# Optimization experiments

Hardware: AMD Instinct MI355X
Metric: run time of the kernel (lower is better)

## Reference

```python
import jax, jax.numpy as jnp
import numpy as np

B, NCH, T = 16, 64, 15000
WS, ST = 500, 250
SR = 250.0
EPS = 1e-06
DM = 512
LN_EPS = 1e-05


def _spectral_constants():
    freqs = np.fft.rfftfreq(WS, d=1.0 / SR).astype(np.float32)  # [F]
    bands = [(1.0, 4.0), (4.0, 8.0), (8.0, 13.0), (13.0, 30.0)]
    bm = np.stack([(freqs >= lo) & (freqs < hi) for lo, hi in bands]).astype(np.float32)  # [4, F]
    bm_norm = bm / bm.sum(axis=1, keepdims=True)  # mean over band bins == matmul with normalized mask
    alpha = ((freqs >= 7.0) & (freqs <= 13.5)).astype(np.float32)  # [F]
    return jnp.asarray(freqs), jnp.asarray(bm_norm), jnp.asarray(alpha)

FREQS, BAND_MASK_NORM, ALPHA_MASK = _spectral_constants()
NUM_FRAMES = (T - WS) // ST + 1
FRAME_IDX = np.arange(NUM_FRAMES)[:, None] * ST + np.arange(WS)[None, :]  # [W, WS]


def _linear_params(k, fin, fout):
    kw, kb = jax.random.split(k)
    W = jax.random.normal(kw, (fin, fout), jnp.float32) * 0.02
    b = jax.random.normal(kb, (fout,), jnp.float32) * 0.01
    return W, b


def setup_inputs() -> dict:
    key = jax.random.key(0)
    ks = jax.random.split(key, 8)
    x = jax.random.normal(ks[0], (B, NCH, T), jnp.float32)
    sensor_pos = jax.random.normal(ks[1], (B, NCH, 2), jnp.float32) * 0.1
    sensor_mask = jax.random.bernoulli(ks[2], 0.9, (B, NCH))
    IN_F = 4 * 3 + 3   # 15
    IN_D = 4 * 2 + 3   # 11
    Wf1, bf1 = _linear_params(ks[3], IN_F, DM)
    Wf2, bf2 = _linear_params(ks[4], DM, DM)
    Wd1, bd1 = _linear_params(ks[5], IN_D, DM)
    Wd2, bd2 = _linear_params(ks[6], DM, DM)
    ln_g = jnp.ones((DM,), jnp.float32)
    ln_b = jnp.zeros((DM,), jnp.float32)
    return {"x": x, "sensor_pos": sensor_pos, "sensor_mask": sensor_mask,
            "Wf1": Wf1, "bf1": bf1, "Wf2": Wf2, "bf2": bf2,
            "ln_g": ln_g, "ln_b": ln_b,
            "Wd1": Wd1, "bd1": bd1, "Wd2": Wd2, "bd2": bd2}


def _mlp(z, W1, b1, W2, b2):
    h = jax.nn.gelu(z @ W1 + b1, approximate=False)
    return h @ W2 + b2


def _layernorm(z, g, b):
    mu = z.mean(-1, keepdims=True)
    var = jnp.var(z, axis=-1, keepdims=True)
    return (z - mu) * jax.lax.rsqrt(var + LN_EPS) * g + b


def _safe_mask(v, fallback):
    return jnp.where(v.any(), v, jnp.full_like(v, fallback))


def _forward(x, sensor_pos, sensor_mask, Wf1, bf1, Wf2, bf2, ln_g, ln_b, Wd1, bd1, Wd2, bd2):
    # frames: [B, W, C, WS]
    frames = x[:, :, FRAME_IDX].transpose(0, 2, 1, 3)
    frames = frames - frames.mean(-1, keepdims=True)
    valid = sensor_mask.astype(frames.dtype)[:, None, :, None]  # [B,1,C,1]
    frames = frames * valid
    spec = jnp.fft.rfft(frames.astype(jnp.float32), axis=-1)
    power = jnp.abs(spec) ** 2 + EPS  # [B,W,C,F]

    # masked band-power means via normalized mask matmul -> [B,W,C,4]
    band_power_t = jnp.einsum('bwcf,kf->bwck', power, BAND_MASK_NORM)
    total_power = jnp.maximum(band_power_t.sum(-1, keepdims=True), EPS)
    rel_power = band_power_t / total_power

    valid_ch = valid  # [B,1,C,1]
    ch_cnt = jnp.maximum(valid_ch.sum(2, keepdims=True), 1.0)
    chan_mean = (band_power_t * valid_ch).sum(2, keepdims=True) / ch_cnt
    topo_dev = jnp.log(jnp.maximum(band_power_t, EPS)) - jnp.log(jnp.maximum(chan_mean, EPS))

    pos_x = sensor_pos[..., 0]
    pos_y = sensor_pos[..., 1]
    left = _safe_mask((pos_x < -0.02) & sensor_mask, False)
    right = _safe_mask((pos_x > 0.02) & sensor_mask, False)
    posterior = _safe_mask((pos_y < -0.02) & sensor_mask, True)
    anterior = _safe_mask((pos_y > 0.02) & sensor_mask, False)

    alpha_power = band_power_t[..., 2]  # [B,W,C]

    def region_mean(m):  # m: [B,C] bool -> [B,W]
        cnt = jnp.maximum(m.sum(-1).astype(alpha_power.dtype), 1.0)[:, None]
        return (alpha_power * m.astype(alpha_power.dtype)[:, None, :]).sum(-1) / cnt

    left_a, right_a = region_mean(left), region_mean(right)
    post_a, ant_a = region_mean(posterior), region_mean(anterior)
    alpha_asym = (left_a - right_a) / jnp.maximum(left_a + right_a + EPS, EPS)
    alpha_ap = (post_a - ant_a) / jnp.maximum(post_a + ant_a + EPS, EPS)
    support = (anterior.sum(-1) > 0) & (posterior.sum(-1) > 0)  # [B]
    alpha_ap = jnp.where(support[:, None], alpha_ap, jnp.zeros_like(alpha_ap))

    alpha_spec = power * ALPHA_MASK  # [B,W,C,F]
    alpha_sum = jnp.maximum(alpha_spec.sum(-1), EPS)
    alpha_peak_freq = (alpha_spec * FREQS).sum(-1) / alpha_sum  # [B,W,C]
    alpha_peak_score = alpha_spec.max(-1) / jnp.maximum(power.mean(-1), EPS)

    log_power = jnp.log(jnp.maximum(band_power_t, EPS))
    channel_ap = jnp.broadcast_to(sensor_pos[:, None, :, 1], alpha_peak_freq.shape)

    features = jnp.concatenate([
        log_power, rel_power, topo_dev,
        alpha_peak_freq[..., None], alpha_peak_score[..., None], channel_ap[..., None],
    ], axis=-1)  # [B,W,C,15]

    ch_cnt2 = jnp.maximum(valid_ch.sum(2), 1.0)  # [B,1,1]
    band_mean = (band_power_t * valid_ch).sum(2) / ch_cnt2       # [B,W,4]
    band_rel_mean = (rel_power * valid_ch).sum(2) / ch_cnt2      # [B,W,4]
    band_log_mean = jnp.log(jnp.maximum(band_mean, EPS))
    delta_theta = band_rel_mean[..., 0] + band_rel_mean[..., 1]
    desc = jnp.concatenate([
        band_log_mean, band_rel_mean,
        jnp.stack([alpha_asym, alpha_ap, delta_theta], axis=-1),
    ], axis=-1)  # [B,W,11]

    tokens = _layernorm(_mlp(features.astype(x.dtype), Wf1, bf1, Wf2, bf2), ln_g, ln_b)
    desc_out = _mlp(desc.astype(x.dtype), Wd1, bd1, Wd2, bd2)
    return tokens, desc_out


def reference(x, sensor_pos, sensor_mask, Wf1, bf1, Wf2, bf2, ln_g, ln_b, Wd1, bd1, Wd2, bd2):
    return _forward(x, sensor_pos, sensor_mask, Wf1, bf1, Wf2, bf2, ln_g, ln_b, Wd1, bd1, Wd2, bd2)
```

## Files before the change

### kernel.cpp

```cpp
#include <hip/hip_runtime.h>
#include <math.h>

#define EPS 1e-6f
#define LN_EPS 1e-5f

typedef __attribute__((ext_vector_type(8))) short bf16x8;
typedef __attribute__((ext_vector_type(4))) float f32x4;

#define SD_OFF    0ULL
#define SD_SZ     (1024ULL*60*128*4)
#define BP_OFF    SD_OFF
#define BTH_OFF   (SD_OFF + 4ULL*1024*1024)
#define BTL_OFF   (BTH_OFF + 65536ULL)
#define FEAT_OFF  (SD_OFF + SD_SZ)
#define FEAT_SZ   (60416ULL*16*4)
#define H_OFF     (FEAT_OFF + FEAT_SZ)
#define H_SZ      (60416ULL*512*2)
#define WT_OFF    (H_OFF + H_SZ)
#define WT_SZ     (512ULL*512*2)
#define DSC_OFF   (WT_OFF + WT_SZ)
#define DSC_SZ    (944ULL*16*4)
#define MSK_OFF   (DSC_OFF + DSC_SZ)
#define MSK_SZ    (1024ULL*4)
#define REG_OFF   (MSK_OFF + MSK_SZ)
#define REG_SZ    (4096ULL*4)
#define CNT_OFF   (REG_OFF + REG_SZ)
#define CNT_SZ    (64ULL*4)
#define SUP_OFF   (CNT_OFF + CNT_SZ)

#define TOKENS_N  30932992ULL

__device__ inline unsigned short f2bf(float f) {
  union { float f; unsigned u; } v; v.f = f;
  unsigned u = v.u;
  return (unsigned short)((u + 0x7fffu + ((u >> 16) & 1u)) >> 16);
}

__device__ inline void gload16(const void* g, void* l) {
  __builtin_amdgcn_global_load_lds((const __attribute__((address_space(1))) unsigned int*)g,
                                   (__attribute__((address_space(3))) unsigned int*)l, 16, 0, 0);
}

__global__ __launch_bounds__(1024) void k_setup(const void* mraw, const float* spos,
    float* maskf, float* regm, float* cnts, float* sup) {
  __shared__ int okint, okflt;
  __shared__ int anyr[4];
  __shared__ float cbuf[4][16];
  int t = threadIdx.x;
  if (t == 0) { okint = 1; okflt = 1; }
  if (t < 4) anyr[t] = 0;
  if (t < 64) cbuf[t>>4][t&15] = 0.f;
  __syncthreads();
  if (t < 256) {
    unsigned v = ((const unsigned*)mraw)[t];
    if (v > 1u) okint = 0;
    if (v != 0u && v != 0x3f800000u) okflt = 0;
  }
  __syncthreads();
  float mv;
  if (okint)      mv = (float)((const int*)mraw)[t];
  else if (okflt) mv = ((const float*)mraw)[t];
  else            mv = (float)((const unsigned char*)mraw)[t];
  maskf[t] = mv;
  bool mk = mv > 0.5f;
  float px = spos[2*t], py = spos[2*t+1];
  int lm = ((px < -0.02f) && mk) ? 1 : 0;
  int rm = ((px >  0.02f) && mk) ? 1 : 0;
  int pm = ((py < -0.02f) && mk) ? 1 : 0;
  int am = ((py >  0.02f) && mk) ? 1 : 0;
  if (lm) anyr[0] = 1;
  if (rm) anyr[1] = 1;
  if (pm) anyr[2] = 1;
  if (am) anyr[3] = 1;
  __syncthreads();
  float lv = anyr[0] ? (float)lm : 0.f;
  float rv = anyr[1] ? (float)rm : 0.f;
  float pv = anyr[2] ? (float)pm : 1.f;
  float av = anyr[3] ? (float)am : 0.f;
  regm[t] = lv; regm[1024+t] = rv; regm[2048+t] = pv; regm[3072+t] = av;
  int b = t >> 6;
  atomicAdd(&cbuf[0][b], lv);
  atomicAdd(&cbuf[1][b], rv);
  atomicAdd(&cbuf[2][b], pv);
  atomicAdd(&cbuf[3][b], av);
  __syncthreads();
  if (t < 64) cnts[t] = cbuf[t>>4][t&15];
  if (t < 16) sup[t] = (cbuf[3][t] > 0.f && cbuf[2][t] > 0.f) ? 1.f : 0.f;
}

__global__ __launch_bounds__(256) void k_wt(const float* Wf2, unsigned short* Wt) {
  __shared__ float tile[64][65];
  int tx = threadIdx.x & 63, ty = threadIdx.x >> 6;
  int k0 = blockIdx.x * 64, n0 = blockIdx.y * 64;
  for (int r = ty; r < 64; r += 4)
    tile[r][tx] = Wf2[(size_t)(k0 + r)*512 + n0 + tx];
  __syncthreads();
  for (int r = ty; r < 64; r += 4)
    Wt[(size_t)(n0 + r)*512 + k0 + tx] = f2bf(tile[tx][r]);
}

__global__ __launch_bounds__(256) void k_twid(unsigned short* FBh, unsigned short* FBl) {
  int col = blockIdx.x, k = threadIdx.x;
  float w = 0.f;
  if (k < 250) {
    if (col < 116) {
      int kk = (col >> 1) + 2;
      int km = (kk * k) % 500;
      float ang = (float)km * 0.012566370614359172f;
      w = (col & 1) ? sinf(ang) : cosf(ang);
    } else if (col == 116) w = (k & 1) ? -1.f : 1.f;
    else if (col == 117) w = 1.f;
  }
  unsigned u = __float_as_uint(w);
  float hf = __uint_as_float(u & 0xffff0000u);
  float r = w - hf;
  int ni2 = col >> 6, nf = (col >> 4) & 3, r15 = col & 15;
  int kt = k >> 5, lg4 = (k >> 3) & 3, e = k & 7;
  int idx = ((((kt*2 + ni2)*4 + nf)*64) + (lg4*16 + r15))*8 + e;
  FBh[idx] = (unsigned short)(u >> 16);
  FBl[idx] = (unsigned short)(__float_as_uint(r) >> 16);
}

__global__ __launch_bounds__(256) void k_dft(const float* __restrict__ x, const float* maskf,
    const unsigned short* __restrict__ FBh, const unsigned short* __restrict__ FBl,
    float* __restrict__ bpg) {
  int c = blockIdx.x, b = blockIdx.y;
  int bc = b*64 + c;
  __shared__ __align__(16) float xs[15360];
  __shared__ float Ep[64][4];
  int t = threadIdx.x;
  float mvv = maskf[bc];
  const float4* xp4 = (const float4*)(x + (size_t)bc*15000);
  float4* xs4 = (float4*)xs;
  for (int i = t; i < 3750; i += 256) {
    float4 v = xp4[i];
    v.x *= mvv; v.y *= mvv; v.z *= mvv; v.w *= mvv;
    xs4[i] = v;
  }
  if (t < 90) xs4[3750 + t] = make_float4(0.f, 0.f, 0.f, 0.f);
  __syncthreads();
  if (t < 240) {
    int j = t >> 2, q = t & 3;
    int len = (q < 3) ? 31 : 32;
    const float2* p = (const float2*)(xs + j*250 + q*62);
    float e = 0.f;
    for (int i = 0; i < len; ++i) { float2 v = p[i]; e = fmaf(v.x, v.x, fmaf(v.y, v.y, e)); }
    Ep[j][q] = e;
  }
  int L = t & 63, wv = t >> 6;
  int mi2 = wv >> 1, ni2 = wv & 1;
  int r15 = L & 15, lg4 = L >> 4;
  f32x4 acc[2][4];
#pragma unroll
  for (int mf = 0; mf < 2; ++mf)
#pragma unroll
    for (int nf = 0; nf < 4; ++nf) acc[mf][nf] = (f32x4){0.f,0.f,0.f,0.f};
  int rowA = mi2*32 + r15;
  const unsigned short* fbh0 = FBh + (size_t)(ni2*4*64 + L)*8;
  const unsigned short* fbl0 = FBl + (size_t)(ni2*4*64 + L)*8;
  for (int kt = 0; kt < 8; ++kt) {
    int k0 = kt*32 + lg4*8;
    bf16x8 bh[4], bl[4];
#pragma unroll
    for (int nf = 0; nf < 4; ++nf) {
      bh[nf] = *(const bf16x8*)(fbh0 + (size_t)(kt*8 + nf)*512);
      bl[nf] = *(const bf16x8*)(fbl0 + (size_t)(kt*8 + nf)*512);
    }
    bf16x8 ah[2], al[2];
#pragma unroll
    for (int mf = 0; mf < 2; ++mf) {
      int row = rowA + mf*16;
      if (row > 60) row = 60;
      int base = row*250 + k0;
      float v[8];
#pragma unroll
      for (int p = 0; p < 4; ++p) {
        float2 vv = *(const float2*)(xs + base + 2*p);
        v[2*p] = vv.x; v[2*p+1] = vv.y;
      }
#pragma unroll
      for (int e = 0; e < 8; ++e) {
        unsigned u = __float_as_uint(v[e]);
        float hf = __uint_as_float(u & 0xffff0000u);
        ah[mf][e] = (short)(u >> 16);
        al[mf][e] = (short)(__float_as_uint(v[e] - hf) >> 16);
      }
    }
#pragma unroll
    for (int mf = 0; mf < 2; ++mf)
#pragma unroll
      for (int nf = 0; nf < 4; ++nf) {
        acc[mf][nf] = __builtin_amdgcn_mfma_f32_16x16x32_bf16(ah[mf], bh[nf], acc[mf][nf], 0, 0, 0);
        acc[mf][nf] = __builtin_amdgcn_mfma_f32_16x16x32_bf16(al[mf], bh[nf], acc[mf][nf], 0, 0, 0);
        acc[mf][nf] = __builtin_amdgcn_mfma_f32_16x16x32_bf16(ah[mf], bl[nf], acc[mf][nf], 0, 0, 0);
      }
  }
  __syncthreads();
  float* Ts = xs;
#pragma unroll
  for (int mf = 0; mf < 2; ++mf)
#pragma unroll
    for (int nf = 0; nf < 4; ++nf) {
      int col = ni2*64 + nf*16 + r15;
      int rw = mi2*32 + mf*16 + lg4*4;
#pragma unroll
      for (int q = 0; q < 4; ++q) Ts[(rw + q)*129 + col] = acc[mf][nf][q];
    }
  __syncthreads();
  if (t < 59) {
    int w = t;
    const float* r0 = Ts + w*129;
    const float* r1 = Ts + (w+1)*129;
    float bs0=0,bs1=0,bs2=0,bs3=0, asum=0, afsum=0, amax=0;
#pragma unroll
    for (int i = 0; i < 58; ++i) {
      float sg = (i & 1) ? -1.f : 1.f;
      float tc = fmaf(sg, r1[2*i],   r0[2*i]);
      float ts = fmaf(sg, r1[2*i+1], r0[2*i+1]);
      float P = fmaf(tc, tc, fmaf(ts, ts, EPS));
      if (i < 6) bs0 += P; else if (i < 14) bs1 += P; else if (i < 24) bs2 += P; else bs3 += P;
      if (i >= 12 && i <= 25) { asum += P; afsum = fmaf(P, 0.5f*(float)(i+2), afsum); amax = fmaxf(amax, P); }
    }
    float nyq  = r0[116] + r1[116];
    float ssum = r0[117] + r1[117];
    float en = Ep[w][0]+Ep[w][1]+Ep[w][2]+Ep[w][3] + Ep[w+1][0]+Ep[w+1][1]+Ep[w+1][2]+Ep[w+1][3];
    float E = fmaf(-ssum * (1.f/500.f), ssum, en);
    float pmean = fmaxf(fmaf(500.f, E, nyq*nyq) * (1.f/502.f) + EPS, EPS);
    float bp0 = bs0*(1.f/6.f), bp1 = bs1*(1.f/8.f), bp2 = bs2*(1.f/10.f), bp3 = bs3*(1.f/34.f);
    float afreq  = afsum / fmaxf(asum, EPS);
    float ascore = amax / pmean;
    float4* o = (float4*)(bpg + (((size_t)(b*59 + w))*64 + c)*8);
    o[0] = make_float4(bp0, bp1, bp2, bp3);
    o[1] = make_float4(afreq, ascore, 0.f, 0.f);
  }
}

__global__ __launch_bounds__(64) void k_feat2(const float* __restrict__ bpg, const float* spos,
    const float* maskf, const float* regm, const float* cnts, const float* sup,
    float* feat, float* descb) {
  int w = blockIdx.x, b = blockIdx.y;
  int c = threadIdx.x, bc = b*64 + c;
  size_t bw = (size_t)(b*59 + w);
  const float4* ip = (const float4*)(bpg + (bw*64 + c)*8);
  float4 f0 = ip[0], f1 = ip[1];
  float bp0 = f0.x, bp1 = f0.y, bp2 = f0.z, bp3 = f0.w;
  float tot = fmaxf(bp0+bp1+bp2+bp3, EPS);
  float rl0 = bp0/tot, rl1 = bp1/tot, rl2 = bp2/tot, rl3 = bp3/tot;
  float valid = maskf[bc];
  float vcnt = valid;
  float ch0 = bp0*valid, ch1 = bp1*valid, ch2 = bp2*valid, ch3 = bp3*valid;
  float br0 = rl0*valid, br1 = rl1*valid, br2 = rl2*valid, br3 = rl3*valid;
  float rg0 = bp2*regm[bc], rg1 = bp2*regm[1024+bc], rg2 = bp2*regm[2048+bc], rg3 = bp2*regm[3072+bc];
#pragma unroll
  for (int off = 1; off < 64; off <<= 1) {
    vcnt += __shfl_xor(vcnt, off, 64);
    ch0 += __shfl_xor(ch0, off, 64); ch1 += __shfl_xor(ch1, off, 64);
    ch2 += __shfl_xor(ch2, off, 64); ch3 += __shfl_xor(ch3, off, 64);
    br0 += __shfl_xor(br0, off, 64); br1 += __shfl_xor(br1, off, 64);
    br2 += __shfl_xor(br2, off, 64); br3 += __shfl_xor(br3, off, 64);
    rg0 += __shfl_xor(rg0, off, 64); rg1 += __shfl_xor(rg1, off, 64);
    rg2 += __shfl_xor(rg2, off, 64); rg3 += __shfl_xor(rg3, off, 64);
  }
  float ccnt = fmaxf(vcnt, 1.f);
  float cm0 = ch0/ccnt, cm1 = ch1/ccnt, cm2 = ch2/ccnt, cm3 = ch3/ccnt;
  float lcm0 = logf(fmaxf(cm0,EPS)), lcm1 = logf(fmaxf(cm1,EPS));
  float lcm2 = logf(fmaxf(cm2,EPS)), lcm3 = logf(fmaxf(cm3,EPS));
  float lg0 = logf(fmaxf(bp0,EPS)), lg1 = logf(fmaxf(bp1,EPS));
  float lg2 = logf(fmaxf(bp2,EPS)), lg3 = logf(fmaxf(bp3,EPS));
  float* fr = feat + (bw*64 + c)*16;
  fr[0]=lg0; fr[1]=lg1; fr[2]=lg2; fr[3]=lg3;
  fr[4]=rl0; fr[5]=rl1; fr[6]=rl2; fr[7]=rl3;
  fr[8]=lg0-lcm0; fr[9]=lg1-lcm1; fr[10]=lg2-lcm2; fr[11]=lg3-lcm3;
  fr[12]=f1.x;
  fr[13]=f1.y;
  fr[14]=spos[bc*2 + 1];
  if (c == 0) {
    float bR0 = br0/ccnt, bR1 = br1/ccnt, bR2 = br2/ccnt, bR3 = br3/ccnt;
    float Lm = rg0 / fmaxf(cnts[b],      1.f);
    float Rm = rg1 / fmaxf(cnts[16+b],   1.f);
    float Pm = rg2 / fmaxf(cnts[32+b],   1.f);
    float Am = rg3 / fmaxf(cnts[48+b],   1.f);
    float* dr = descb + bw*16;
    dr[0]=lcm0; dr[1]=lcm1; dr[2]=lcm2; dr[3]=lcm3;
    dr[4]=bR0; dr[5]=bR1; dr[6]=bR2; dr[7]=bR3;
    dr[8]=(Lm - Rm) / fmaxf(Lm + Rm + EPS, EPS);
    dr[9]=(sup[b] > 0.5f) ? (Pm - Am) / fmaxf(Pm + Am + EPS, EPS) : 0.f;
    dr[10]=bR0 + bR1;
  }
}

__global__ __launch_bounds__(256) void k_mlp1(const float* feat, const float* Wf1, const float* bf1,
                                              unsigned short* h) {
  int w = blockIdx.x, b = blockIdx.y;
  __shared__ float Wsh[15*512];
  __shared__ float b1s[512];
  __shared__ float fsh[64*16];
  int t = threadIdx.x;
  for (int i = t; i < 15*512; i += 256) Wsh[i] = Wf1[i];
  for (int i = t; i < 512; i += 256) b1s[i] = bf1[i];
  const float* fb = feat + (size_t)(b*59 + w)*64*16;
  for (int i = t; i < 1024; i += 256) fsh[i] = fb[i];
  __syncthreads();
  int j0 = t*2, j1 = t*2 + 1;
  float w0[15], w1[15];
#pragma unroll
  for (int k = 0; k < 15; ++k) { w0[k] = Wsh[k*512+j0]; w1[k] = Wsh[k*512+j1]; }
  float bb0 = b1s[j0], bb1 = b1s[j1];
  unsigned short* hb = h + (size_t)(b*59 + w)*64*512;
  for (int r = 0; r < 64; ++r) {
    float a0 = bb0, a1 = bb1;
#pragma unroll
    for (int k = 0; k < 15; ++k) { float f = fsh[r*16+k]; a0 = fmaf(f, w0[k], a0); a1 = fmaf(f, w1[k], a1); }
    float g0 = 0.5f * a0 * (1.f + erff(a0 * 0.70710678118654752f));
    float g1 = 0.5f * a1 * (1.f + erff(a1 * 0.70710678118654752f));
    ((unsigned int*)(hb + r*512))[t] = (unsigned)f2bf(g0) | ((unsigned)f2bf(g1) << 16);
  }
}

__global__ __launch_bounds__(256, 2) void k_mlp2(const unsigned short* h, const unsigned short* Wt,
    const float* bf2, const float* lng, const float* lnb, float* out) {
  __shared__ __align__(16) unsigned short As[64*32];
  __shared__ __align__(16) unsigned short Bs[512*32];
  __shared__ float red[64][4][2];
  __shared__ float lnp[64][2];
  int t = threadIdx.x;
  int L = t & 63, wvid = t >> 6;
  int row0 = blockIdx.x * 64;
  int arow = t >> 2;
  int akc  = (t & 3) ^ ((t >> 3) & 3);
  const unsigned short* hsrc = h + (size_t)(row0 + arow)*512 + akc*8;
  f32x4 acc[4][8];
#pragma unroll
  for (int m = 0; m < 4; ++m)
#pragma unroll
    for (int n = 0; n < 8; ++n) acc[m][n] = (f32x4){0.f,0.f,0.f,0.f};
  int r15 = L & 15, lg4 = L >> 4;
  int swz = (r15 >> 1) & 3;
  int kca = lg4 ^ swz;
  int aoff = r15*32 + kca*8;
  int boff = (wvid*128 + r15)*32 + kca*8;
  for (int kt = 0; kt < 16; ++kt) {
    gload16(hsrc + kt*32, (char*)As + t*16);
#pragma unroll
    for (int r = 0; r < 8; ++r) {
      int n = r*256 + t;
      int col = n >> 2;
      int kc = (n & 3) ^ ((n >> 3) & 3);
      gload16(Wt + (size_t)col*512 + kt*32 + kc*8, (char*)Bs + n*16);
    }
    __syncthreads();
    bf16x8 av[4], bv[8];
#pragma unroll
    for (int m = 0; m < 4; ++m) av[m] = *(const bf16x8*)&As[aoff + m*512];
#pragma unroll
    for (int n = 0; n < 8; ++n) bv[n] = *(const bf16x8*)&Bs[boff + n*512];
#pragma unroll
    for (int m = 0; m < 4; ++m)
#pragma unroll
      for (int n = 0; n < 8; ++n)
        acc[m][n] = __builtin_amdgcn_mfma_f32_16x16x32_bf16(av[m], bv[n], acc[m][n], 0, 0, 0);
    __syncthreads();
  }
  float b2v[8], gv[8], btv[8];
#pragma unroll
  for (int n = 0; n < 8; ++n) {
    int col = wvid*128 + n*16 + r15;
    b2v[n] = bf2[col]; gv[n] = lng[col]; btv[n] = lnb[col];
  }
  float s1[4][4], s2[4][4];
#pragma unroll
  for (int m = 0; m < 4; ++m)
#pragma unroll
    for (int r = 0; r < 4; ++r) { s1[m][r] = 0.f; s2[m][r] = 0.f; }
#pragma unroll
  for (int m = 0; m < 4; ++m)
#pragma unroll
    for (int n = 0; n < 8; ++n)
#pragma unroll
      for (int r = 0; r < 4; ++r) {
        float z = acc[m][n][r] + b2v[n];
        acc[m][n][r] = z;
        s1[m][r] += z;
        s2[m][r] = fmaf(z, z, s2[m][r]);
      }
#pragma unroll
  for (int off = 1; off < 16; off <<= 1)
#pragma unroll
    for (int m = 0; m < 4; ++m)
#pragma unroll
      for (int r = 0; r < 4; ++r) {
        s1[m][r] += __shfl_xor(s1[m][r], off, 64);
        s2[m][r] += __shfl_xor(s2[m][r], off, 64);
      }
  if (r15 == 0) {
#pragma unroll
    for (int m = 0; m < 4; ++m)
#pragma unroll
      for (int r = 0; r < 4; ++r) {
        int rw = m*16 + lg4*4 + r;
        red[rw][wvid][0] = s1[m][r];
        red[rw][wvid][1] = s2[m][r];
      }
  }
  __syncthreads();
  if (t < 64) {
    float a = red[t][0][0] + red[t][1][0] + red[t][2][0] + red[t][3][0];
    float q = red[t][0][1] + red[t][1][1] + red[t][2][1] + red[t][3][1];
    float mu = a * (1.f/512.f);
    float var = q * (1.f/512.f) - mu*mu;
    lnp[t][0] = mu;
    lnp[t][1] = rsqrtf(var + LN_EPS);
  }
  __syncthreads();
  float* ob = out + (size_t)row0*512;
#pragma unroll
  for (int m = 0; m < 4; ++m)
#pragma unroll
    for (int r = 0; r < 4; ++r) {
      int rw = m*16 + lg4*4 + r;
      float mu = lnp[rw][0], rs = lnp[rw][1];
#pragma unroll
      for (int n = 0; n < 8; ++n) {
        int col = wvid*128 + n*16 + r15;
        ob[(size_t)rw*512 + col] = fmaf((acc[m][n][r] - mu)*rs, gv[n], btv[n]);
      }
    }
}

__global__ __launch_bounds__(256) void k_desc(const float* descb, const float* Wd1, const float* bd1,
    const float* Wd2, const float* bd2, float* out) {
  int blk = blockIdx.x;
  int cq = blockIdx.y;
  __shared__ float ds[16][12];
  __shared__ float hd[16*512];
  int t = threadIdx.x;
  { int r = t >> 4, cc = t & 15;
    if (cc < 11) ds[r][cc] = descb[(size_t)(blk*16 + r)*16 + cc]; }
  __syncthreads();
  {
    int c0 = t, c1 = t + 256;
    float wa[11], wb[11];
#pragma unroll
    for (int k = 0; k < 11; ++k) { wa[k] = Wd1[k*512+c0]; wb[k] = Wd1[k*512+c1]; }
    float ba = bd1[c0], bb = bd1[c1];
    for (int r = 0; r < 16; ++r) {
      float a0 = ba, a1 = bb;
#pragma unroll
      for (int k = 0; k < 11; ++k) { float f = ds[r][k]; a0 = fmaf(f, wa[k], a0); a1 = fmaf(f, wb[k], a1); }
      hd[r*512+c0] = 0.5f * a0 * (1.f + erff(a0 * 0.70710678118654752f));
      hd[r*512+c1] = 0.5f * a1 * (1.f + erff(a1 * 0.70710678118654752f));
    }
  }
  __syncthreads();
  int col = cq*128 + (t & 127);
  int half = t >> 7;
  float accv[8];
  float bz = bd2[col];
#pragma unroll
  for (int r = 0; r < 8; ++r) accv[r] = bz;
  for (int k4 = 0; k4 < 128; ++k4) {
    float w0 = Wd2[(size_t)(k4*4+0)*512 + col];
    float w1 = Wd2[(size_t)(k4*4+1)*512 + col];
    float w2 = Wd2[(size_t)(k4*4+2)*512 + col];
    float w3 = Wd2[(size_t)(k4*4+3)*512 + col];
#pragma unroll
    for (int r = 0; r < 8; ++r) {
      float4 hv = *(const float4*)&hd[(half*8+r)*512 + k4*4];
      accv[r] = fmaf(hv.x, w0, fmaf(hv.y, w1, fmaf(hv.z, w2, fmaf(hv.w, w3, accv[r]))));
    }
  }
  float* ob = out + TOKENS_N;
#pragma unroll
  for (int r = 0; r < 8; ++r) {
    int grow = blk*16 + half*8 + r;
    ob[(size_t)grow*512 + col] = accv[r];
  }
}

extern "C" void kernel_launch(void* const* d_in, const int* in_sizes, int n_in,
                              void* d_out, int out_size, void* d_ws, size_t ws_size,
                              hipStream_t stream) {
  (void)in_sizes; (void)n_in; (void)out_size; (void)ws_size;
  const float* x    = (const float*)d_in[0];
  const float* spos = (const float*)d_in[1];
  const void*  mask = d_in[2];
  const float* Wf1  = (const float*)d_in[3];
  const float* bf1  = (const float*)d_in[4];
  const float* Wf2  = (const float*)d_in[5];
  const float* bf2  = (const float*)d_in[6];
  const float* lng  = (const float*)d_in[7];
  const float* lnb  = (const float*)d_in[8];
  const float* Wd1  = (const float*)d_in[9];
  const float* bd1  = (const float*)d_in[10];
  const float* Wd2  = (const float*)d_in[11];
  const float* bd2  = (const float*)d_in[12];
  char* ws = (char*)d_ws;
  float*          bpg   = (float*)(ws + BP_OFF);
  unsigned short* FBh   = (unsigned short*)(ws + BTH_OFF);
  unsigned short* FBl   = (unsigned short*)(ws + BTL_OFF);
  float*          feat  = (float*)(ws + FEAT_OFF);
  unsigned short* h     = (unsigned short*)(ws + H_OFF);
  unsigned short* Wt    = (unsigned short*)(ws + WT_OFF);
  float*          descb = (float*)(ws + DSC_OFF);
  float*          maskf = (float*)(ws + MSK_OFF);
  float*          regm  = (float*)(ws + REG_OFF);
  float*          cnts  = (float*)(ws + CNT_OFF);
  float*          sup   = (float*)(ws + SUP_OFF);
  float*          out   = (float*)d_out;

  hipLaunchKernelGGL(k_setup,  dim3(1),      dim3(1024), 0, stream, mask, spos, maskf, regm, cnts, sup);
  hipLaunchKernelGGL(k_wt,     dim3(8,8),    dim3(256),  0, stream, Wf2, Wt);
  hipLaunchKernelGGL(k_twid,   dim3(128),    dim3(256),  0, stream, FBh, FBl);
  hipLaunchKernelGGL(k_dft,    dim3(64,16),  dim3(256),  0, stream, x, maskf, FBh, FBl, bpg);
  hipLaunchKernelGGL(k_feat2,  dim3(59,16),  dim3(64),   0, stream, bpg, spos, maskf, regm, cnts, sup, feat, descb);
  hipLaunchKernelGGL(k_mlp1,   dim3(59,16),  dim3(256),  0, stream, feat, Wf1, bf1, h);
  hipLaunchKernelGGL(k_mlp2,   dim3(944),    dim3(256),  0, stream, h, Wt, bf2, lng, lnb, out);
  hipLaunchKernelGGL(k_desc,   dim3(59,4),   dim3(256),  0, stream, descb, Wd1, bd1, Wd2, bd2, out);
}
```

Measured before the change: 380.1 us.

## Fuse first MLP layer and GELU into second GEMM kernel via split-bf16 MFMA

Removes the separate k_mlp1 kernel and its 60k×512 bf16 hidden buffer. The token kernel now computes each 32-column slice of the first layer on the fly, using MFMA with hi/lo bf16 splits of the features and Wf1 (three products) to stay close to fp32 accuracy. GELU is applied in registers and the result is written straight into the swizzled A tile in shared memory. This saves about 62 MB of global writes and reads, at the cost of extra MFMA and erf work inside the main GEMM loop, plus a small prep kernel that converts Wf1 into the MFMA operand layout.

```diff
diff --git a/kernel.cpp b/kernel.cpp
--- a/kernel.cpp
+++ b/kernel.cpp
@@ -14,9 +14,9 @@
 #define BTL_OFF   (BTH_OFF + 65536ULL)
 #define FEAT_OFF  (SD_OFF + SD_SZ)
 #define FEAT_SZ   (60416ULL*16*4)
-#define H_OFF     (FEAT_OFF + FEAT_SZ)
-#define H_SZ      (60416ULL*512*2)
-#define WT_OFF    (H_OFF + H_SZ)
+#define W1H_OFF   (FEAT_OFF + FEAT_SZ)
+#define W1L_OFF   (W1H_OFF + 32768ULL)
+#define WT_OFF    (W1L_OFF + 32768ULL)
 #define WT_SZ     (512ULL*512*2)
 #define DSC_OFF   (WT_OFF + WT_SZ)
 #define DSC_SZ    (944ULL*16*4)
@@ -97,6 +97,18 @@
   __syncthreads();
   for (int r = ty; r < 64; r += 4)
     Wt[(size_t)(n0 + r)*512 + k0 + tx] = f2bf(tile[tx][r]);
+}
+
+__global__ __launch_bounds__(256) void k_w1(const float* Wf1, unsigned short* W1h, unsigned short* W1l) {
+  int id = blockIdx.x*256 + threadIdx.x;
+  int col = id & 511, k = id >> 9;
+  float w = (k < 15) ? Wf1[k*512 + col] : 0.f;
+  unsigned u = __float_as_uint(w);
+  float hf = __uint_as_float(u & 0xffff0000u);
+  float r = w - hf;
+  int idx = (((col >> 4)*4 + (k >> 3))*16 + (col & 15))*8 + (k & 7);
+  W1h[idx] = (unsigned short)(u >> 16);
+  W1l[idx] = (unsigned short)(__float_as_uint(r) >> 16);
 }
 
 __global__ __launch_bounds__(256) void k_twid(unsigned short* FBh, unsigned short* FBl) {
@@ -274,6 +286,7 @@
   fr[12]=f1.x;
   fr[13]=f1.y;
   fr[14]=spos[bc*2 + 1];
+  fr[15]=0.f;
   if (c == 0) {
     float bR0 = br0/ccnt, bR1 = br1/ccnt, bR2 = br2/ccnt, bR3 = br3/ccnt;
     float Lm = rg0 / fmaxf(cnts[b],      1.f);
@@ -289,64 +302,88 @@
   }
 }
 
-__global__ __launch_bounds__(256) void k_mlp1(const float* feat, const float* Wf1, const float* bf1,
-                                              unsigned short* h) {
-  int w = blockIdx.x, b = blockIdx.y;
-  __shared__ float Wsh[15*512];
-  __shared__ float b1s[512];
-  __shared__ float fsh[64*16];
-  int t = threadIdx.x;
-  for (int i = t; i < 15*512; i += 256) Wsh[i] = Wf1[i];
-  for (int i = t; i < 512; i += 256) b1s[i] = bf1[i];
-  const float* fb = feat + (size_t)(b*59 + w)*64*16;
-  for (int i = t; i < 1024; i += 256) fsh[i] = fb[i];
-  __syncthreads();
-  int j0 = t*2, j1 = t*2 + 1;
-  float w0[15], w1[15];
-#pragma unroll
-  for (int k = 0; k < 15; ++k) { w0[k] = Wsh[k*512+j0]; w1[k] = Wsh[k*512+j1]; }
-  float bb0 = b1s[j0], bb1 = b1s[j1];
-  unsigned short* hb = h + (size_t)(b*59 + w)*64*512;
-  for (int r = 0; r < 64; ++r) {
-    float a0 = bb0, a1 = bb1;
-#pragma unroll
-    for (int k = 0; k < 15; ++k) { float f = fsh[r*16+k]; a0 = fmaf(f, w0[k], a0); a1 = fmaf(f, w1[k], a1); }
-    float g0 = 0.5f * a0 * (1.f + erff(a0 * 0.70710678118654752f));
-    float g1 = 0.5f * a1 * (1.f + erff(a1 * 0.70710678118654752f));
-    ((unsigned int*)(hb + r*512))[t] = (unsigned)f2bf(g0) | ((unsigned)f2bf(g1) << 16);
-  }
-}
-
-__global__ __launch_bounds__(256, 2) void k_mlp2(const unsigned short* h, const unsigned short* Wt,
+__global__ __launch_bounds__(256, 2) void k_tok(const float* __restrict__ feat,
+    const unsigned short* __restrict__ W1h, const unsigned short* __restrict__ W1l,
+    const float* __restrict__ bf1, const unsigned short* __restrict__ Wt,
     const float* bf2, const float* lng, const float* lnb, float* out) {
   __shared__ __align__(16) unsigned short As[64*32];
   __shared__ __align__(16) unsigned short Bs[512*32];
+  __shared__ float b1s[512];
   __shared__ float red[64][4][2];
   __shared__ float lnp[64][2];
   int t = threadIdx.x;
   int L = t & 63, wvid = t >> 6;
   int row0 = blockIdx.x * 64;
-  int arow = t >> 2;
-  int akc  = (t & 3) ^ ((t >> 3) & 3);
-  const unsigned short* hsrc = h + (size_t)(row0 + arow)*512 + akc*8;
+  int r15 = L & 15, lg4 = L >> 4;
+  if (t < 256) { b1s[t] = bf1[t]; b1s[256+t] = bf1[256+t]; }
+  bf16x8 a1h = (bf16x8){0,0,0,0,0,0,0,0}, a1l = (bf16x8){0,0,0,0,0,0,0,0};
+  {
+    int row = row0 + wvid*16 + r15;
+    if (lg4 < 2) {
+      const float4* fp = (const float4*)(feat + (size_t)row*16 + lg4*8);
+      float4 v0 = fp[0], v1 = fp[1];
+      float v[8] = {v0.x, v0.y, v0.z, v0.w, v1.x, v1.y, v1.z, v1.w};
+#pragma unroll
+      for (int e = 0; e < 8; ++e) {
+        unsigned u = __float_as_uint(v[e]);
+        float hf = __uint_as_float(u & 0xffff0000u);
+        a1h[e] = (short)(u >> 16);
+        a1l[e] = (short)(__float_as_uint(v[e] - hf) >> 16);
+      }
+    }
+  }
   f32x4 acc[4][8];
 #pragma unroll
   for (int m = 0; m < 4; ++m)
 #pragma unroll
     for (int n = 0; n < 8; ++n) acc[m][n] = (f32x4){0.f,0.f,0.f,0.f};
-  int r15 = L & 15, lg4 = L >> 4;
   int swz = (r15 >> 1) & 3;
   int kca = lg4 ^ swz;
   int aoff = r15*32 + kca*8;
   int boff = (wvid*128 + r15)*32 + kca*8;
+  __syncthreads();
   for (int kt = 0; kt < 16; ++kt) {
-    gload16(hsrc + kt*32, (char*)As + t*16);
 #pragma unroll
     for (int r = 0; r < 8; ++r) {
       int n = r*256 + t;
       int col = n >> 2;
       int kc = (n & 3) ^ ((n >> 3) & 3);
       gload16(Wt + (size_t)col*512 + kt*32 + kc*8, (char*)Bs + n*16);
+    }
+    f32x4 acc1[2];
+    acc1[0] = (f32x4){0.f,0.f,0.f,0.f};
+    acc1[1] = (f32x4){0.f,0.f,0.f,0.f};
+#pragma unroll
+    for (int n2 = 0; n2 < 2; ++n2) {
+      const unsigned short* wb = W1h + (size_t)(kt*2 + n2)*512 + L*8;
+      const unsigned short* wl = W1l + (size_t)(kt*2 + n2)*512 + L*8;
+      bf16x8 b1h = *(const bf16x8*)wb;
+      bf16x8 b1l = *(const bf16x8*)wl;
+      acc1[n2] = __builtin_amdgcn_mfma_f32_16x16x32_bf16(a1h, b1h, acc1[n2], 0, 0, 0);
+      acc1[n2] = __builtin_amdgcn_mfma_f32_16x16x32_bf16(a1l, b1h, acc1[n2], 0, 0, 0);
+      acc1[n2] = __builtin_amdgcn_mfma_f32_16x16x32_bf16(a1h, b1l, acc1[n2], 0, 0, 0);
+    }
+    unsigned short hv[8];
+#pragma unroll
+    for (int n2 = 0; n2 < 2; ++n2) {
+      float bb = b1s[kt*32 + n2*16 + r15];
+#pragma unroll
+      for (int q = 0; q < 4; ++q) {
+        float z = acc1[n2][q] + bb;
+        float g = 0.5f * z * (1.f + erff(z * 0.70710678118654752f));
+        hv[n2*4 + q] = f2bf(g);
+      }
+    }
+#pragma unroll
+    for (int n2 = 0; n2 < 2; ++n2) {
+      int col5 = n2*16 + r15;
+      int cb = col5 >> 3;
+#pragma unroll
+      for (int q = 0; q < 4; ++q) {
+        int rw = wvid*16 + lg4*4 + q;
+        int kcs = cb ^ ((rw >> 1) & 3);
+        As[rw*32 + kcs*8 + (col5 & 7)] = hv[n2*4 + q];
+      }
     }
     __syncthreads();
     bf16x8 av[4], bv[8];
@@ -499,7 +536,8 @@
   unsigned short* FBh   = (unsigned short*)(ws + BTH_OFF);
   unsigned short* FBl   = (unsigned short*)(ws + BTL_OFF);
   float*          feat  = (float*)(ws + FEAT_OFF);
-  unsigned short* h     = (unsigned short*)(ws + H_OFF);
+  unsigned short* W1h   = (unsigned short*)(ws + W1H_OFF);
+  unsigned short* W1l   = (unsigned short*)(ws + W1L_OFF);
   unsigned short* Wt    = (unsigned short*)(ws + WT_OFF);
   float*          descb = (float*)(ws + DSC_OFF);
   float*          maskf = (float*)(ws + MSK_OFF);
@@ -510,10 +548,10 @@
 
   hipLaunchKernelGGL(k_setup,  dim3(1),      dim3(1024), 0, stream, mask, spos, maskf, regm, cnts, sup);
   hipLaunchKernelGGL(k_wt,     dim3(8,8),    dim3(256),  0, stream, Wf2, Wt);
+  hipLaunchKernelGGL(k_w1,     dim3(64),     dim3(256),  0, stream, Wf1, W1h, W1l);
   hipLaunchKernelGGL(k_twid,   dim3(128),    dim3(256),  0, stream, FBh, FBl);
   hipLaunchKernelGGL(k_dft,    dim3(64,16),  dim3(256),  0, stream, x, maskf, FBh, FBl, bpg);
   hipLaunchKernelGGL(k_feat2,  dim3(59,16),  dim3(64),   0, stream, bpg, spos, maskf, regm, cnts, sup, feat, descb);
-  hipLaunchKernelGGL(k_mlp1,   dim3(59,16),  dim3(256),  0, stream, feat, Wf1, bf1, h);
-  hipLaunchKernelGGL(k_mlp2,   dim3(944),    dim3(256),  0, stream, h, Wt, bf2, lng, lnb, out);
+  hipLaunchKernelGGL(k_tok,    dim3(944),    dim3(256),  0, stream, feat, W1h, W1l, bf1, Wt, bf2, lng, lnb, out);
   hipLaunchKernelGGL(k_desc,   dim3(59,4),   dim3(256),  0, stream, descb, Wd1, bd1, Wd2, bd2, out);
 }
```

Result: faster. 345.3 us (-9.2%).
